# Performance work log

Measured on AMD Instinct MI355X. Metric: run time of the kernel, lower is better.

Reference implementation:

```python
import jax, jax.numpy as jnp
import numpy as np

N = 262144   # number of occupied voxels (sparse points)
C = 64       # channels
G = 128
K = 27       # 3x3x3 kernel offsets


def _build_kernel_map(rng):
    # Unique occupied voxel coordinates on a G^3 grid.
    flat = rng.choice(G ** 3, size=N, replace=False)
    order = np.argsort(flat)
    skeys = flat[order]
    coords = np.stack(np.unravel_index(flat, (G, G, G)), axis=1).astype(np.int64)  # [N,3]
    offsets = np.array([[dx, dy, dz] for dx in (-1, 0, 1) for dy in (-1, 0, 1) for dz in (-1, 0, 1)], np.int64)
    nb = np.full((N, K), -1, np.int32)  # -1 == no neighbor at this offset
    for k in range(K):
        nc = coords + offsets[k]
        valid = np.all((nc >= 0) & (nc < G), axis=1)
        nkey = (nc[:, 0] * G + nc[:, 1]) * G + nc[:, 2]
        pos = np.clip(np.searchsorted(skeys, nkey), 0, N - 1)
        hit = valid & (skeys[pos] == nkey)
        nb[hit, k] = order[pos[hit]].astype(np.int32)
    return nb


def setup_inputs() -> dict:
    nb = _build_kernel_map(np.random.default_rng(0))
    key = jax.random.key(0)
    k1, k2, k3, k4, k5 = jax.random.split(key, 5)
    feat = jax.random.normal(k1, (N, C), jnp.float32)
    W = jax.random.normal(k2, (C, C), jnp.float32) / np.float32(np.sqrt(C))   # 1x1 bottleneck weight
    b1 = jax.random.normal(k3, (C,), jnp.float32) * 0.01                      # bottleneck bias
    dw = jax.random.normal(k4, (K, C), jnp.float32) / np.float32(np.sqrt(K))  # channelwise 3^3 kernel
    b2 = jax.random.normal(k5, (C,), jnp.float32) * 0.01                      # channelwise bias
    return {"feat": feat, "neighbor_idx": jnp.asarray(nb), "W": W, "b1": b1, "b2": b2, "dw": dw}


def reference(feat, neighbor_idx, W, b1, b2, dw):
    # bottleneck: 1x1 sparse conv == pointwise linear over features
    bx = feat @ W + b1  # [N,C]
    mask = neighbor_idx >= 0
    safe = jnp.where(mask, neighbor_idx, 0)
    # channelwise (depthwise) 3x3x3 sparse conv: sum over 27 offsets of
    # gathered neighbor features times per-channel weight. scan over the
    # fixed 27 offsets to avoid a [N,27,C] intermediate.
    def body(acc, inp):
        wk, idxk, mk = inp  # [C], [N], [N]
        g = jnp.where(mk[:, None], bx[idxk], 0.0)
        return acc + g * wk, None
    acc, _ = jax.lax.scan(body, jnp.zeros_like(bx), (dw, safe.T, mask.T))
    # residual add (note: the module never applies its ReLU in forward)
    return feat + acc + b2
```

## Files before the change

### kernel.cpp

```cpp
#include <hip/hip_runtime.h>
#include <hip/hip_bf16.h>

#define NPTS 262144
#define NC 64
#define NK 27

typedef __attribute__((ext_vector_type(8))) short bf16x8;
typedef __attribute__((ext_vector_type(4))) float f32x4;

__device__ __forceinline__ float bflo(unsigned u) { return __uint_as_float(u << 16); }
__device__ __forceinline__ float bfhi(unsigned u) { return __uint_as_float(u & 0xffff0000u); }

__device__ __forceinline__ unsigned cvtpk(float lo, float hi) {
    unsigned r;
    asm("v_cvt_pk_bf16_f32 %0, %1, %2" : "=v"(r) : "v"(lo), "v"(hi));
    return r;
}

union BF { unsigned u[4]; bf16x8 v; };


__global__ __launch_bounds__(256) void gemm_mfma(const float* __restrict__ feat,
                                                 const float* __restrict__ W,
                                                 const float* __restrict__ b1,
                                                 ushort* __restrict__ bx) {
    __shared__ float Ws[NC * NC];
    __shared__ float b1S[NC];
    int t = threadIdx.x;
#pragma unroll
    for (int i = 0; i < 4; ++i)
        ((float4*)Ws)[t + i * 256] = ((const float4*)W)[t + i * 256];
    if (t < NC) b1S[t] = b1[t];
    __syncthreads();

    int lane = t & 63;
    int col = lane & 15;
    int kg = lane >> 4;
    int wid = blockIdx.x * 4 + (t >> 6);
    const int NWAVES = 2048 * 4;
    const int NTILES = NPTS / 16;

    BF Bf[2][4];
#pragma unroll
    for (int ks = 0; ks < 2; ++ks)
#pragma unroll
        for (int ct = 0; ct < 4; ++ct)
#pragma unroll
            for (int r = 0; r < 4; ++r) {
                float lo = Ws[(ks * 32 + kg * 8 + 2 * r) * NC + ct * 16 + col];
                float hi = Ws[(ks * 32 + kg * 8 + 2 * r + 1) * NC + ct * 16 + col];
                Bf[ks][ct].u[r] = cvtpk(lo, hi);
            }
    float bias[4];
#pragma unroll
    for (int ct = 0; ct < 4; ++ct) bias[ct] = b1S[ct * 16 + col];

    for (int tile = wid; tile < NTILES; tile += NWAVES) {
        long r0 = (long)tile * 16;
        const float* ap = feat + (r0 + col) * NC + kg * 8;
        float4 a0 = *(const float4*)(ap);
        float4 a1 = *(const float4*)(ap + 4);
        float4 a2 = *(const float4*)(ap + 32);
        float4 a3 = *(const float4*)(ap + 36);
        BF A0, A1;
        A0.u[0] = cvtpk(a0.x, a0.y); A0.u[1] = cvtpk(a0.z, a0.w);
        A0.u[2] = cvtpk(a1.x, a1.y); A0.u[3] = cvtpk(a1.z, a1.w);
        A1.u[0] = cvtpk(a2.x, a2.y); A1.u[1] = cvtpk(a2.z, a2.w);
        A1.u[2] = cvtpk(a3.x, a3.y); A1.u[3] = cvtpk(a3.z, a3.w);

        f32x4 acc[4];
#pragma unroll
        for (int ct = 0; ct < 4; ++ct) {
            acc[ct] = (f32x4){bias[ct], bias[ct], bias[ct], bias[ct]};
            acc[ct] = __builtin_amdgcn_mfma_f32_16x16x32_bf16(A0.v, Bf[0][ct].v, acc[ct], 0, 0, 0);
            acc[ct] = __builtin_amdgcn_mfma_f32_16x16x32_bf16(A1.v, Bf[1][ct].v, acc[ct], 0, 0, 0);
        }

#pragma unroll
        for (int i = 0; i < 4; ++i) {
            uint* bu = (uint*)(bx + (r0 + kg * 4 + i) * NC);
            bu[col]      = cvtpk(acc[0][i], acc[1][i]);
            bu[16 + col] = cvtpk(acc[2][i], acc[3][i]);
        }
    }
}

__global__ __launch_bounds__(256, 8) void dwconv(const float* __restrict__ feat,
                                                 const int* __restrict__ nb,
                                                 const float* __restrict__ b2,
                                                 const float* __restrict__ dw,
                                                 const ushort* __restrict__ bx,
                                                 float* __restrict__ out) {
    __shared__ float dwS[28 * NC];
    __shared__ float b2S[NC];
    __shared__ int nbS[32 * NK];
    int t = threadIdx.x;
    for (int i = t; i < NK * NC; i += 256) {
        int p = i & 63;
        int ch = ((p >> 1) & 15) + ((p & 1) << 4) + (p & 32);
        dwS[i] = dw[(i & ~63) + ch];
    }
    if (t < NC) dwS[27 * NC + t] = 0.f;
    if (t < NC) b2S[t] = b2[t];

    int b = blockIdx.x;
    int chunk = gridDim.x >> 3;
    int sb = (b & 7) * chunk + (b >> 3);

    const uint4* nbsrc = (const uint4*)(nb + (size_t)sb * 32 * NK);
    if (t < 216) ((uint4*)nbS)[t] = nbsrc[t];
    __syncthreads();

    int r = t >> 3;
    int q = t & 7;
    long row = (long)sb * 32 + r;
    int lo_c0 = (q < 4) ? 4 * q : 16 + 4 * q;
    int hi_c0 = lo_c0 + 16;

    float4 flo = *(const float4*)(feat + row * NC + lo_c0);
    float4 fhi = *(const float4*)(feat + row * NC + hi_c0);

    float acc[8] = {0.f, 0.f, 0.f, 0.f, 0.f, 0.f, 0.f, 0.f};

    const int* nrow = nbS + r * NK;
    const ushort* bq = bx + q * 8;
    const float* wq = dwS + q * 8;

#pragma unroll
    for (int k = 0; k < NK; ++k) {
        int id = nrow[k];
        int ids = max(id, 0);
        int krow = (id < 0) ? 27 : k;
        uint4 g = *(const uint4*)(bq + (size_t)ids * NC);
        float4 w0 = *(const float4*)(wq + krow * NC);
        float4 w1 = *(const float4*)(wq + krow * NC + 4);
        acc[0] += bflo(g.x) * w0.x;
        acc[1] += bfhi(g.x) * w0.y;
        acc[2] += bflo(g.y) * w0.z;
        acc[3] += bfhi(g.y) * w0.w;
        acc[4] += bflo(g.z) * w1.x;
        acc[5] += bfhi(g.z) * w1.y;
        acc[6] += bflo(g.w) * w1.z;
        acc[7] += bfhi(g.w) * w1.w;
    }

    float4 olo = make_float4(acc[0] + flo.x + b2S[lo_c0 + 0],
                             acc[2] + flo.y + b2S[lo_c0 + 1],
                             acc[4] + flo.z + b2S[lo_c0 + 2],
                             acc[6] + flo.w + b2S[lo_c0 + 3]);
    float4 ohi = make_float4(acc[1] + fhi.x + b2S[hi_c0 + 0],
                             acc[3] + fhi.y + b2S[hi_c0 + 1],
                             acc[5] + fhi.z + b2S[hi_c0 + 2],
                             acc[7] + fhi.w + b2S[hi_c0 + 3]);
    *(float4*)(out + row * NC + lo_c0) = olo;
    *(float4*)(out + row * NC + hi_c0) = ohi;
}

extern "C" void kernel_launch(void* const* d_in, const int* in_sizes, int n_in,
                              void* d_out, int out_size, void* d_ws, size_t ws_size,
                              hipStream_t stream) {
    const float* feat = (const float*)d_in[0];
    const int*   nb   = (const int*)d_in[1];
    const float* W    = (const float*)d_in[2];
    const float* b1   = (const float*)d_in[3];
    const float* b2   = (const float*)d_in[4];
    const float* dw   = (const float*)d_in[5];
    float* out = (float*)d_out;
    ushort* bx = (ushort*)d_ws;

    gemm_mfma<<<2048, 256, 0, stream>>>(feat, W, b1, bx);
    dwconv<<<NPTS / 32, 256, 0, stream>>>(feat, nb, b2, dw, bx, out);
}
```

Baseline: 205.3 us.

## Process four rows per thread in dwconv with sentinel zero row and packed FMA

The depthwise conv kernel now handles 128 rows per block, with each thread covering four rows. The neighbor table is transposed in LDS so four indices load as one int4, which raises memory-level parallelism with four independent gathers per offset and reuses each weight load across the four rows. Missing neighbors are redirected to a zeroed sentinel row written by the GEMM kernel when the workspace is large enough, which removes the per-element masking; a masked fallback path covers the other case. Packed f32x2 math is used for the multiply-adds. In exchange, register pressure rises (launch bounds drop to 5 waves), and the grid has fewer blocks.

```diff
diff --git a/kernel.cpp b/kernel.cpp
--- a/kernel.cpp
+++ b/kernel.cpp
@@ -4,18 +4,24 @@
 #define NPTS 262144
 #define NC 64
 #define NK 27
+#define RPB 128
+#define NBS 132
 
 typedef __attribute__((ext_vector_type(8))) short bf16x8;
 typedef __attribute__((ext_vector_type(4))) float f32x4;
-
-__device__ __forceinline__ float bflo(unsigned u) { return __uint_as_float(u << 16); }
-__device__ __forceinline__ float bfhi(unsigned u) { return __uint_as_float(u & 0xffff0000u); }
+typedef __attribute__((ext_vector_type(2))) float f32x2;
 
 __device__ __forceinline__ unsigned cvtpk(float lo, float hi) {
     unsigned r;
     asm("v_cvt_pk_bf16_f32 %0, %1, %2" : "=v"(r) : "v"(lo), "v"(hi));
     return r;
 }
+__device__ __forceinline__ f32x2 up2(unsigned u) {
+    f32x2 r;
+    r.x = __uint_as_float(u << 16);
+    r.y = __uint_as_float(u & 0xffff0000u);
+    return r;
+}
 
 union BF { unsigned u[4]; bf16x8 v; };
 
@@ -23,10 +29,12 @@
 __global__ __launch_bounds__(256) void gemm_mfma(const float* __restrict__ feat,
                                                  const float* __restrict__ W,
                                                  const float* __restrict__ b1,
-                                                 ushort* __restrict__ bx) {
+                                                 ushort* __restrict__ bx,
+                                                 uint* __restrict__ zrow) {
     __shared__ float Ws[NC * NC];
     __shared__ float b1S[NC];
     int t = threadIdx.x;
+    if (zrow && blockIdx.x == 0 && t < 32) zrow[t] = 0u;
 #pragma unroll
     for (int i = 0; i < 4; ++i)
         ((float4*)Ws)[t + i * 256] = ((const float4*)W)[t + i * 256];
@@ -75,7 +83,6 @@
             acc[ct] = __builtin_amdgcn_mfma_f32_16x16x32_bf16(A0.v, Bf[0][ct].v, acc[ct], 0, 0, 0);
             acc[ct] = __builtin_amdgcn_mfma_f32_16x16x32_bf16(A1.v, Bf[1][ct].v, acc[ct], 0, 0, 0);
         }
-
 #pragma unroll
         for (int i = 0; i < 4; ++i) {
             uint* bu = (uint*)(bx + (r0 + kg * 4 + i) * NC);
@@ -85,75 +92,105 @@
     }
 }
 
-__global__ __launch_bounds__(256, 8) void dwconv(const float* __restrict__ feat,
+template <bool SENT>
+__global__ __launch_bounds__(256, 5) void dwconv(const float* __restrict__ feat,
                                                  const int* __restrict__ nb,
                                                  const float* __restrict__ b2,
                                                  const float* __restrict__ dw,
                                                  const ushort* __restrict__ bx,
                                                  float* __restrict__ out) {
-    __shared__ float dwS[28 * NC];
+    __shared__ int nbT[NK * NBS];
+    __shared__ float dwS[NK * NC];
     __shared__ float b2S[NC];
-    __shared__ int nbS[32 * NK];
     int t = threadIdx.x;
     for (int i = t; i < NK * NC; i += 256) {
         int p = i & 63;
         int ch = ((p >> 1) & 15) + ((p & 1) << 4) + (p & 32);
         dwS[i] = dw[(i & ~63) + ch];
     }
-    if (t < NC) dwS[27 * NC + t] = 0.f;
     if (t < NC) b2S[t] = b2[t];
 
     int b = blockIdx.x;
     int chunk = gridDim.x >> 3;
     int sb = (b & 7) * chunk + (b >> 3);
 
-    const uint4* nbsrc = (const uint4*)(nb + (size_t)sb * 32 * NK);
-    if (t < 216) ((uint4*)nbS)[t] = nbsrc[t];
+    const int* nsrc = nb + (size_t)sb * RPB * NK;
+    for (int i = t; i < RPB * NK; i += 256) {
+        int r = i / NK;
+        int k = i - r * NK;
+        int v = nsrc[i];
+        if (SENT) v = (v < 0) ? NPTS : v;
+        nbT[k * NBS + r] = v;
+    }
     __syncthreads();
 
-    int r = t >> 3;
+    int g = t >> 3;
     int q = t & 7;
-    long row = (long)sb * 32 + r;
+    long row0 = (long)sb * RPB + g * 4;
+    unsigned qo = (unsigned)q << 4;
+
+    f32x2 acc[4][4];
+#pragma unroll
+    for (int j = 0; j < 4; ++j)
+#pragma unroll
+        for (int i = 0; i < 4; ++i) acc[j][i] = (f32x2){0.f, 0.f};
+
+    const char* bp = (const char*)bx;
+    const int* nbase = nbT + g * 4;
+    const f32x2* wbase = (const f32x2*)dwS + q * 4;
+
+#pragma unroll 3
+    for (int k = 0; k < NK; ++k) {
+        int4 idx = *(const int4*)(nbase + k * NBS);
+        int sx = idx.x, sy = idx.y, sz = idx.z, sw = idx.w;
+        if (!SENT) { sx = max(sx, 0); sy = max(sy, 0); sz = max(sz, 0); sw = max(sw, 0); }
+        uint4 g0 = *(const uint4*)(bp + (((unsigned)sx << 7) + qo));
+        uint4 g1 = *(const uint4*)(bp + (((unsigned)sy << 7) + qo));
+        uint4 g2 = *(const uint4*)(bp + (((unsigned)sz << 7) + qo));
+        uint4 g3 = *(const uint4*)(bp + (((unsigned)sw << 7) + qo));
+        if (!SENT) {
+            unsigned m0 = idx.x >= 0 ? 0xffffffffu : 0u;
+            unsigned m1 = idx.y >= 0 ? 0xffffffffu : 0u;
+            unsigned m2 = idx.z >= 0 ? 0xffffffffu : 0u;
+            unsigned m3 = idx.w >= 0 ? 0xffffffffu : 0u;
+            g0.x &= m0; g0.y &= m0; g0.z &= m0; g0.w &= m0;
+            g1.x &= m1; g1.y &= m1; g1.z &= m1; g1.w &= m1;
+            g2.x &= m2; g2.y &= m2; g2.z &= m2; g2.w &= m2;
+            g3.x &= m3; g3.y &= m3; g3.z &= m3; g3.w &= m3;
+        }
+        f32x2 w0 = wbase[k * 32 + 0];
+        f32x2 w1 = wbase[k * 32 + 1];
+        f32x2 w2 = wbase[k * 32 + 2];
+        f32x2 w3 = wbase[k * 32 + 3];
+        acc[0][0] += up2(g0.x) * w0; acc[0][1] += up2(g0.y) * w1;
+        acc[0][2] += up2(g0.z) * w2; acc[0][3] += up2(g0.w) * w3;
+        acc[1][0] += up2(g1.x) * w0; acc[1][1] += up2(g1.y) * w1;
+        acc[1][2] += up2(g1.z) * w2; acc[1][3] += up2(g1.w) * w3;
+        acc[2][0] += up2(g2.x) * w0; acc[2][1] += up2(g2.y) * w1;
+        acc[2][2] += up2(g2.z) * w2; acc[2][3] += up2(g2.w) * w3;
+        acc[3][0] += up2(g3.x) * w0; acc[3][1] += up2(g3.y) * w1;
+        acc[3][2] += up2(g3.z) * w2; acc[3][3] += up2(g3.w) * w3;
+    }
+
     int lo_c0 = (q < 4) ? 4 * q : 16 + 4 * q;
     int hi_c0 = lo_c0 + 16;
-
-    float4 flo = *(const float4*)(feat + row * NC + lo_c0);
-    float4 fhi = *(const float4*)(feat + row * NC + hi_c0);
-
-    float acc[8] = {0.f, 0.f, 0.f, 0.f, 0.f, 0.f, 0.f, 0.f};
-
-    const int* nrow = nbS + r * NK;
-    const ushort* bq = bx + q * 8;
-    const float* wq = dwS + q * 8;
-
-#pragma unroll
-    for (int k = 0; k < NK; ++k) {
-        int id = nrow[k];
-        int ids = max(id, 0);
-        int krow = (id < 0) ? 27 : k;
-        uint4 g = *(const uint4*)(bq + (size_t)ids * NC);
-        float4 w0 = *(const float4*)(wq + krow * NC);
-        float4 w1 = *(const float4*)(wq + krow * NC + 4);
-        acc[0] += bflo(g.x) * w0.x;
-        acc[1] += bfhi(g.x) * w0.y;
-        acc[2] += bflo(g.y) * w0.z;
-        acc[3] += bfhi(g.y) * w0.w;
-        acc[4] += bflo(g.z) * w1.x;
-        acc[5] += bfhi(g.z) * w1.y;
-        acc[6] += bflo(g.w) * w1.z;
-        acc[7] += bfhi(g.w) * w1.w;
-    }
-
-    float4 olo = make_float4(acc[0] + flo.x + b2S[lo_c0 + 0],
-                             acc[2] + flo.y + b2S[lo_c0 + 1],
-                             acc[4] + flo.z + b2S[lo_c0 + 2],
-                             acc[6] + flo.w + b2S[lo_c0 + 3]);
-    float4 ohi = make_float4(acc[1] + fhi.x + b2S[hi_c0 + 0],
-                             acc[3] + fhi.y + b2S[hi_c0 + 1],
-                             acc[5] + fhi.z + b2S[hi_c0 + 2],
-                             acc[7] + fhi.w + b2S[hi_c0 + 3]);
-    *(float4*)(out + row * NC + lo_c0) = olo;
-    *(float4*)(out + row * NC + hi_c0) = ohi;
+#pragma unroll
+    for (int j = 0; j < 4; ++j) {
+        long row = row0 + j;
+        const float* fp = feat + row * NC;
+        float4 flo = *(const float4*)(fp + lo_c0);
+        float4 fhi = *(const float4*)(fp + hi_c0);
+        float4 olo = make_float4(acc[j][0].x + flo.x + b2S[lo_c0 + 0],
+                                 acc[j][1].x + flo.y + b2S[lo_c0 + 1],
+                                 acc[j][2].x + flo.z + b2S[lo_c0 + 2],
+                                 acc[j][3].x + flo.w + b2S[lo_c0 + 3]);
+        float4 ohi = make_float4(acc[j][0].y + fhi.x + b2S[hi_c0 + 0],
+                                 acc[j][1].y + fhi.y + b2S[hi_c0 + 1],
+                                 acc[j][2].y + fhi.z + b2S[hi_c0 + 2],
+                                 acc[j][3].y + fhi.w + b2S[hi_c0 + 3]);
+        *(float4*)(out + row * NC + lo_c0) = olo;
+        *(float4*)(out + row * NC + hi_c0) = ohi;
+    }
 }
 
 extern "C" void kernel_launch(void* const* d_in, const int* in_sizes, int n_in,
@@ -168,6 +205,12 @@
     float* out = (float*)d_out;
     ushort* bx = (ushort*)d_ws;
 
-    gemm_mfma<<<2048, 256, 0, stream>>>(feat, W, b1, bx);
-    dwconv<<<NPTS / 32, 256, 0, stream>>>(feat, nb, b2, dw, bx, out);
-}
+    bool sent = ws_size >= (size_t)(NPTS + 1) * NC * sizeof(ushort);
+    uint* zrow = sent ? (uint*)(bx + (size_t)NPTS * NC) : nullptr;
+
+    gemm_mfma<<<2048, 256, 0, stream>>>(feat, W, b1, bx, zrow);
+    if (sent)
+        dwconv<true><<<NPTS / RPB, 256, 0, stream>>>(feat, nb, b2, dw, bx, out);
+    else
+        dwconv<false><<<NPTS / RPB, 256, 0, stream>>>(feat, nb, b2, dw, bx, out);
+}
```

Measured after the change: 204.8 us. Within noise of the previous version (-0.2%).
